# Kernel optimization log

Measured on AMD Instinct MI355X. Metric: run time of the kernel, lower is better.

The kernel has to match this reference:

```python
import jax, jax.numpy as jnp
from jax import lax
import numpy as np

NEIGHBORS = ((1, 3), (0, 2, 4), (1, 5), (0, 4, 6), (1, 3, 5, 7), (2, 4, 8), (3, 7), (4, 6, 8), (5, 7))
EDGE_SRC = np.array([s for t, ns in enumerate(NEIGHBORS) for s in ns])  # 25 edges
EDGE_DST = np.array([t for t, ns in enumerate(NEIGHBORS) for _ in ns])
NE = len(EDGE_SRC)  # 25
NG, SP = 9, 64      # num_grids, single_plane = 576 // 9
R, C_IN, C_OUT, ROI = 64, 256, 576, 14
GN_GROUPS = 36
EPS = 1e-5


def conv2d(x, w, b, stride, pad):
    y = lax.conv_general_dilated(x, w, (stride, stride), [(pad, pad), (pad, pad)],
                                 dimension_numbers=('NCHW', 'OIHW', 'NCHW'))
    return y + b[None, :, None, None]


def group_norm(x, groups, gamma, beta):
    B, C, H, W = x.shape
    xg = x.reshape(B, groups, -1)
    mu = xg.mean(-1, keepdims=True)
    var = xg.var(-1, keepdims=True)
    xn = ((xg - mu) / jnp.sqrt(var + EPS)).reshape(B, C, H, W)
    return xn * gamma[None, :, None, None] + beta[None, :, None, None]


def edge_conv(inp, dw_w, dw_b, pw_w, pw_b):
    # depthwise 5x5 (groups=SP) then pointwise 1x1
    y = lax.conv_general_dilated(inp, dw_w, (1, 1), [(2, 2), (2, 2)],
                                 dimension_numbers=('NCHW', 'OIHW', 'NCHW'),
                                 feature_group_count=SP) + dw_b[None, :, None, None]
    return jnp.einsum('bchw,oc->bohw', y, pw_w) + pw_b[None, :, None, None]


def deconv_grouped(x, w_t, b, groups):
    # torch ConvTranspose2d(k=4, s=2, p=1, groups) as lhs-dilated conv
    k, s, p = 4, 2, 1
    in_c, out_g = w_t.shape[0], w_t.shape[1]
    in_g = in_c // groups
    w = w_t.reshape(groups, in_g, out_g, k, k).transpose(0, 2, 1, 3, 4).reshape(groups * out_g, in_g, k, k)
    w = jnp.flip(w, (-2, -1))
    y = lax.conv_general_dilated(x, w, (1, 1), [(k - 1 - p, k - 1 - p)] * 2,
                                 lhs_dilation=(s, s),
                                 dimension_numbers=('NCHW', 'OIHW', 'NCHW'),
                                 feature_group_count=groups)
    return y + b[None, :, None, None]


def setup_inputs() -> dict:
    key = jax.random.key(0)
    ks = iter(jax.random.split(key, 32))
    n = lambda shape, s=0.02: jax.random.normal(next(ks), shape, jnp.float32) * s
    inp = {
        'x': jax.random.normal(next(ks), (R, C_IN, ROI, ROI), jnp.float32),
        'convs_w0': n((C_OUT, C_IN, 3, 3)),
        'convs_b0': n((C_OUT,)),
        'convs_w': n((7, C_OUT, C_OUT, 3, 3)),
        'convs_b': n((7, C_OUT)),
        'gn_gamma': jnp.ones((8, C_OUT), jnp.float32),
        'gn_beta': jnp.zeros((8, C_OUT), jnp.float32),
        'fo_dw_w': n((NE, SP, 1, 5, 5), 0.05),
        'fo_dw_b': n((NE, SP)),
        'fo_pw_w': n((NE, SP, SP), 0.05),
        'fo_pw_b': n((NE, SP)),
        'so_dw_w': n((NE, SP, 1, 5, 5), 0.05),
        'so_dw_b': n((NE, SP)),
        'so_pw_w': n((NE, SP, SP), 0.05),
        'so_pw_b': n((NE, SP)),
        'up1_w': n((C_OUT, SP, 4, 4), 0.01),
        'up1_b': jnp.zeros((C_OUT,), jnp.float32),
        'sbn1_gamma': jnp.ones((C_OUT,), jnp.float32),
        'sbn1_beta': jnp.zeros((C_OUT,), jnp.float32),
        'up2_w': n((C_OUT, 1, 4, 4), 0.01),
        'up2_b': jnp.full((NG,), -np.log(0.99 / 0.01), jnp.float32),
    }
    return inp


def reference(x, convs_w0, convs_b0, convs_w, convs_b, gn_gamma, gn_beta,
              fo_dw_w, fo_dw_b, fo_pw_w, fo_pw_b,
              so_dw_w, so_dw_b, so_pw_w, so_pw_b,
              up1_w, up1_b, sbn1_gamma, sbn1_beta, up2_w, up2_b):
    # dense conv stack: stride 2 first, then 7 stride-1 convs (GN + ReLU each)
    h = jax.nn.relu(group_norm(conv2d(x, convs_w0, convs_b0, 2, 1), GN_GROUPS, gn_gamma[0], gn_beta[0]))
    for i in range(7):
        h = jax.nn.relu(group_norm(conv2d(h, convs_w[i], convs_b[i], 1, 1),
                                   GN_GROUPS, gn_gamma[i + 1], gn_beta[i + 1]))
    B, _, Hh, Wh = h.shape  # [B, 576, 7, 7]
    xg = h.reshape(B, NG, SP, Hh, Wh).transpose(1, 0, 2, 3, 4)  # [9, B, 64, 7, 7]
    # first-order message passing over 25 grid edges
    msgs1 = jax.vmap(edge_conv)(xg[EDGE_SRC], fo_dw_w, fo_dw_b, fo_pw_w, fo_pw_b)
    first = xg + jax.ops.segment_sum(msgs1, EDGE_DST, num_segments=NG)
    # second-order message passing (sources are first-order features)
    msgs2 = jax.vmap(edge_conv)(first[EDGE_SRC], so_dw_w, so_dw_b, so_pw_w, so_pw_b)
    second = xg + jax.ops.segment_sum(msgs2, EDGE_DST, num_segments=NG)
    x2 = second.transpose(1, 0, 2, 3, 4).reshape(B, NG * SP, Hh, Wh)

    def head(t):
        t = deconv_grouped(t, up1_w, up1_b, NG)           # [B, 576, 14, 14]
        t = jax.nn.relu(group_norm(t, NG, sbn1_gamma, sbn1_beta))
        return deconv_grouped(t, up2_w, up2_b, NG)        # [B, 9, 28, 28]

    return (head(h), head(x2))
```

## Files before the change

kernel.cpp:

```cpp
#include <hip/hip_runtime.h>
#include <hip/hip_bf16.h>

#define BB 64
#define CIN 256
#define CC 576
#define NGR 9
#define SPC 64
#define HW7 49
#define HW14 196
#define HW28 784

__device__ __constant__ int EDGE_SRC_C[24] = {1,3, 0,2,4, 1,5, 0,4,6, 1,3,5,7, 2,4,8, 3,7, 4,6,8, 5,7};
__device__ __constant__ int EDGE_OFF_C[9]  = {0,2,5,7,10,14,17,19,22};
__device__ __constant__ int EDGE_CNT_C[9]  = {2,3,2,3,4,3,2,3,2};

static __device__ __forceinline__ float bf2f(__hip_bfloat16 v){ return __bfloat162float(v); }
static __device__ __forceinline__ __hip_bfloat16 f2bf(float v){ return __float2bfloat16(v); }
static __device__ __forceinline__ float ldin(const void* p, size_t i, int isbf){
  return isbf ? bf2f(((const __hip_bfloat16*)p)[i]) : ((const float*)p)[i];
}

using bfrag = __attribute__((ext_vector_type(8))) short;
using f32x4 = __attribute__((ext_vector_type(4))) float;

__global__ void detect_kernel(const unsigned short* xs, int* flag) {
  if (threadIdx.x==0 && blockIdx.x==0) {
    int plaus = 0;
    for (int i=0;i<64;i++){
      unsigned short u = xs[2*i];
      int e = (u>>7)&0xFF;
      if (e>=100 && e<=140) plaus++;
    }
    *flag = (plaus >= 40) ? 1 : 0;
  }
}

__global__ __launch_bounds__(256) void xcvt_kernel(
    const void* __restrict__ x, const int* __restrict__ flagp,
    __hip_bfloat16* __restrict__ act0) {
  const int b = blockIdx.x, icb = blockIdx.y, pxb = blockIdx.z, t = threadIdx.x;
  const int isbf = *flagp;
  __shared__ float lds[32][29];
  for (int idx=t; idx<32*28; idx+=256){
    int i = idx/28, j = idx - i*28;
    lds[i][j] = ldin(x, ((size_t)b*CIN + icb*32+i)*HW14 + pxb*28 + j, isbf);
  }
  __syncthreads();
  for (int idx=t; idx<28*32; idx+=256){
    int j = idx >> 5, i = idx & 31;
    act0[((size_t)b*HW14 + pxb*28 + j)*CIN + icb*32 + i] = f2bf(lds[i][j]);
  }
}

__global__ __launch_bounds__(256) void wcvt0_kernel(
    const void* __restrict__ w, const int* __restrict__ flagp,
    __hip_bfloat16* __restrict__ dst) {
  const int oc = blockIdx.x, t = threadIdx.x;
  const int isbf = *flagp;
  __shared__ float lds[2304];
  for (int idx=t; idx<2304; idx+=256)
    lds[idx] = ldin(w, (size_t)oc*2304 + idx, isbf);
  __syncthreads();
  for (int idx=t; idx<2304; idx+=256){
    int koff = idx >> 8, rem = idx & 255;
    int icb = rem >> 5, ici = rem & 31;
    dst[(((size_t)koff*8 + icb)*CC + oc)*32 + ici] = f2bf(lds[rem*9 + koff]);
  }
}

__global__ __launch_bounds__(256) void wcvtL_kernel(
    const void* __restrict__ w, int li, const int* __restrict__ flagp,
    __hip_bfloat16* __restrict__ dst) {
  const int oc = blockIdx.x, t = threadIdx.x;
  const int isbf = *flagp;
  __shared__ float lds[5184];
  for (int idx=t; idx<5184; idx+=256)
    lds[idx] = ldin(w, ((size_t)li*CC + oc)*5184 + idx, isbf);
  __syncthreads();
  for (int idx=t; idx<5184; idx+=256){
    int koff = idx / 576, rem = idx - koff*576;
    int icb = rem >> 5, ici = rem & 31;
    dst[(((size_t)koff*18 + icb)*CC + oc)*32 + ici] = f2bf(lds[rem*9 + koff]);
  }
}

static __device__ __forceinline__ void epilogue_gn(
    float* s_out, float* s_stats, const f32x4 (&acc)[2][2],
    int wm, int wn, int ln, int quad, int t,
    const void* bias, int bias_off,
    const void* gamma, const void* beta, int goff,
    int nbb, int isbf, int b,
    __hip_bfloat16* __restrict__ out)
{
  __syncthreads();
  #pragma unroll
  for (int nf=0; nf<2; nf++){
    int chl = wn*32 + nf*16 + ln;
    float bv = ldin(bias, (size_t)bias_off + nbb + chl, isbf);
    #pragma unroll
    for (int mf=0; mf<2; mf++){
      #pragma unroll
      for (int r=0; r<4; r++){
        int px = wm*32 + mf*16 + quad*4 + r;
        s_out[chl*65 + px] = acc[mf][nf][r] + bv;
      }
    }
  }
  __syncthreads();
  {
    int wv = t >> 6, l = t & 63;
    float s=0.f, ss=0.f;
    for (int j=l; j<784; j+=64){
      int cq = j/49, px = j - cq*49;
      float v = s_out[(wv*16+cq)*65 + px];
      s += v; ss += v*v;
    }
    #pragma unroll
    for (int o=32;o>0;o>>=1){ s+=__shfl_down(s,o); ss+=__shfl_down(ss,o); }
    if (l==0){
      float mean=s/784.f, var=ss/784.f-mean*mean;
      s_stats[wv*2]=mean; s_stats[wv*2+1]=rsqrtf(fmaxf(var,0.f)+1e-5f);
    }
  }
  __syncthreads();
  for (int idx=t; idx<392; idx+=256){
    int px = idx>>3, ck = idx&7;
    alignas(16) __hip_bfloat16 tmp[8];
    #pragma unroll
    for (int u=0;u<8;u++){
      int chl = ck*8+u;
      int gi = chl>>4;
      float ga = ldin(gamma, (size_t)goff + nbb + chl, isbf);
      float be = ldin(beta,  (size_t)goff + nbb + chl, isbf);
      float v = (s_out[chl*65+px]-s_stats[gi*2])*s_stats[gi*2+1]*ga + be;
      tmp[u] = f2bf(fmaxf(v,0.f));
    }
    *(bfrag*)(out + ((size_t)b*64+px)*CC + nbb + ck*8) = *(const bfrag*)tmp;
  }
}

__global__ __launch_bounds__(256) void conv3_v3_kernel(
    const __hip_bfloat16* __restrict__ A,
    const __hip_bfloat16* __restrict__ Wb,
    const void* __restrict__ bias, int bias_off,
    const void* __restrict__ gamma, const void* __restrict__ beta, int goff,
    const int* __restrict__ flagp,
    __hip_bfloat16* __restrict__ out) {
  const int t = threadIdx.x;
  const int l = t & 63, w = t >> 6;
  const int wm = w & 1, wn = (w >> 1) & 1;
  const int ln = l & 15, quad = l >> 4;
  const int b = blockIdx.x, nbb = blockIdx.y*32;
  const int isbf = *flagp;

  __shared__ alignas(16) char smem[8320];
  __shared__ float s_stats[4];
  __hip_bfloat16* sA0 = (__hip_bfloat16*)smem;
  __hip_bfloat16* sA1 = (__hip_bfloat16*)(smem + 4000);
  float* s_out = (float*)smem;

  if (t < 8){
    bfrag z = {0,0,0,0,0,0,0,0};
    __hip_bfloat16* sb = (t<4)? sA0 : sA1;
    *(bfrag*)(sb + 49*40 + (t&3)*8) = z;
  }

  int r0a[9], r1a[9];
  {
    int p0 = wm*32 + ln, p1 = p0+16;
    int y0=p0/7, x0=p0-y0*7, y1=p1/7, x1=p1-y1*7;
    bool v0=p0<49, v1=p1<49;
    #pragma unroll
    for (int koff=0;koff<9;koff++){
      int dy=koff/3-1, dx=koff-(koff/3)*3-1;
      int sy0=y0+dy,sx0=x0+dx, sy1=y1+dy,sx1=x1+dx;
      r0a[koff] = (v0&&sy0>=0&&sy0<7&&sx0>=0&&sx0<7)? sy0*7+sx0 : 49;
      r1a[koff] = (v1&&sy1>=0&&sy1<7&&sx1>=0&&sx1<7)? sy1*7+sx1 : 49;
    }
  }

  f32x4 acc2[2];
  acc2[0] = (f32x4){0.f,0.f,0.f,0.f};
  acc2[1] = (f32x4){0.f,0.f,0.f,0.f};

  const int px_s = t>>2, ic_s = (t&3)*8;
  const __hip_bfloat16* Abase = A + ((size_t)b*64 + px_s)*CC + ic_s;

  if (t<196) *(bfrag*)(sA0 + px_s*40 + ic_s) = *(const bfrag*)(Abase);
  __syncthreads();

  const int nidx = nbb + wn*16 + ln;
  for (int icb=0; icb<18; icb++){
    __hip_bfloat16* curb = (icb&1)? sA1 : sA0;
    if (icb<17 && t<196){
      __hip_bfloat16* nxtb = (icb&1)? sA0 : sA1;
      *(bfrag*)(nxtb + px_s*40 + ic_s) = *(const bfrag*)(Abase + (icb+1)*32);
    }
    const __hip_bfloat16* wpB = Wb + (size_t)icb*18432 + (size_t)nidx*32 + quad*8;
    #pragma unroll
    for (int koff=0;koff<9;koff++){
      bfrag a0 = *(const bfrag*)(curb + r0a[koff]*40 + quad*8);
      bfrag a1 = *(const bfrag*)(curb + r1a[koff]*40 + quad*8);
      bfrag b0 = *(const bfrag*)(wpB + (size_t)koff*331776);
      acc2[0] = __builtin_amdgcn_mfma_f32_16x16x32_bf16(a0, b0, acc2[0], 0,0,0);
      acc2[1] = __builtin_amdgcn_mfma_f32_16x16x32_bf16(a1, b0, acc2[1], 0,0,0);
    }
    __syncthreads();
  }

  {
    const int chl = wn*16 + ln;
    float bv = ldin(bias, (size_t)bias_off + nbb + chl, isbf);
    #pragma unroll
    for (int mf=0; mf<2; mf++)
      #pragma unroll
      for (int r=0;r<4;r++){
        int px = wm*32 + mf*16 + quad*4 + r;
        s_out[chl*65 + px] = acc2[mf][r] + bv;
      }
  }
  __syncthreads();
  {
    int wv = t >> 6, l2 = t & 63;
    if (wv < 2){
      float s=0.f, ss=0.f;
      for (int j=l2; j<784; j+=64){
        int cq = j/49, px = j - cq*49;
        float v = s_out[(wv*16+cq)*65 + px];
        s += v; ss += v*v;
      }
      #pragma unroll
      for (int o=32;o>0;o>>=1){ s+=__shfl_down(s,o); ss+=__shfl_down(ss,o); }
      if (l2==0){
        float mean=s/784.f, var=ss/784.f-mean*mean;
        s_stats[wv*2]=mean; s_stats[wv*2+1]=rsqrtf(fmaxf(var,0.f)+1e-5f);
      }
    }
  }
  __syncthreads();
  if (t < 196){
    int px = t>>2, ck = t&3;
    alignas(16) __hip_bfloat16 tmp[8];
    #pragma unroll
    for (int u=0;u<8;u++){
      int chl = ck*8+u;
      int gi = chl>>4;
      float ga = ldin(gamma, (size_t)goff + nbb + chl, isbf);
      float be = ldin(beta,  (size_t)goff + nbb + chl, isbf);
      float v = (s_out[chl*65+px]-s_stats[gi*2])*s_stats[gi*2+1]*ga + be;
      tmp[u] = f2bf(fmaxf(v,0.f));
    }
    *(bfrag*)(out + ((size_t)b*64+px)*CC + nbb + ck*8) = *(const bfrag*)tmp;
  }
}

__global__ __launch_bounds__(256) void conv0_fused_kernel(
    const __hip_bfloat16* __restrict__ A,
    const __hip_bfloat16* __restrict__ Wb,
    const void* __restrict__ bias,
    const void* __restrict__ gamma, const void* __restrict__ beta,
    const int* __restrict__ flagp,
    __hip_bfloat16* __restrict__ out) {
  const int t = threadIdx.x;
  const int l = t & 63, w = t >> 6;
  const int wm = w & 1, wn = w >> 1;
  const int ln = l & 15, quad = l >> 4;
  const int b = blockIdx.x, nbb = blockIdx.y*64;

  __shared__ alignas(16) __hip_bfloat16 sC[197*40];
  __shared__ alignas(16) float s_out_arr[64*65];
  __shared__ float s_stats[8];

  if (t < 4){
    bfrag z = {0,0,0,0,0,0,0,0};
    *(bfrag*)(sC + 196*40 + t*8) = z;
  }

  int yy[2], xx[2]; bool pv[2];
  #pragma unroll
  for (int mf=0; mf<2; mf++){
    int p = wm*32 + mf*16 + ln;
    pv[mf] = p<49; yy[mf]=p/7; xx[mf]=p-yy[mf]*7;
  }

  f32x4 acc[2][2];
  #pragma unroll
  for (int i=0;i<2;i++)
    #pragma unroll
    for (int j=0;j<2;j++) acc[i][j] = (f32x4){0.f,0.f,0.f,0.f};

  for (int icb=0; icb<8; icb++){
    __syncthreads();
    for (int idx=t*8; idx<6272; idx+=2048){
      int px = idx>>5, ic = idx&31;
      *(bfrag*)(sC + px*40 + ic) = *(const bfrag*)(A + ((size_t)b*196+px)*256 + icb*32 + ic);
    }
    __syncthreads();
    for (int koff=0; koff<9; koff++){
      const int dy = koff/3 - 1, dx = koff - (koff/3)*3 - 1;
      int sy0=2*yy[0]+dy, sx0=2*xx[0]+dx;
      int r0 = (pv[0]&&sy0>=0&&sy0<14&&sx0>=0&&sx0<14) ? sy0*14+sx0 : 196;
      int sy1=2*yy[1]+dy, sx1=2*xx[1]+dx;
      int r1 = (pv[1]&&sy1>=0&&sy1<14&&sx1>=0&&sx1<14) ? sy1*14+sx1 : 196;
      bfrag a0 = *(const bfrag*)(sC + r0*40 + quad*8);
      bfrag a1 = *(const bfrag*)(sC + r1*40 + quad*8);
      const __hip_bfloat16* wp = Wb + ((size_t)(koff*8+icb)*576 + nbb + wn*32 + ln)*32 + quad*8;
      bfrag b0 = *(const bfrag*)(wp);
      bfrag b1 = *(const bfrag*)(wp + 16*32);
      acc[0][0] = __builtin_amdgcn_mfma_f32_16x16x32_bf16(a0, b0, acc[0][0], 0,0,0);
      acc[1][0] = __builtin_amdgcn_mfma_f32_16x16x32_bf16(a1, b0, acc[1][0], 0,0,0);
      acc[0][1] = __builtin_amdgcn_mfma_f32_16x16x32_bf16(a0, b1, acc[0][1], 0,0,0);
      acc[1][1] = __builtin_amdgcn_mfma_f32_16x16x32_bf16(a1, b1, acc[1][1], 0,0,0);
    }
  }

  epilogue_gn(s_out_arr, s_stats, acc, wm, wn, ln, quad, t,
              bias, 0, gamma, beta, 0, nbb, *flagp, b, out);
}

__global__ __launch_bounds__(256) void dw_edge_kernel(
    const __hip_bfloat16* __restrict__ F,
    const void* __restrict__ dw_w,
    const void* __restrict__ dw_b,
    const int* __restrict__ flagp,
    __hip_bfloat16* __restrict__ Y) {
  const int b = blockIdx.x, e = blockIdx.y, t = threadIdx.x;
  const int isbf = *flagp;
  const int src = EDGE_SRC_C[e];
  __shared__ alignas(16) __hip_bfloat16 sA[50*72];
  for (int idx=t; idx<400; idx+=256){
    if (idx < 392){
      int px = idx>>3, ic = (idx&7)*8;
      *(bfrag*)(sA + px*72 + ic) = *(const bfrag*)(F + ((size_t)b*64+px)*CC + src*64 + ic);
    } else {
      bfrag z = {0,0,0,0,0,0,0,0};
      *(bfrag*)(sA + 49*72 + (idx-392)*8) = z;
    }
  }
  __syncthreads();
  const int ch = t & 63, wv = t >> 6;
  float wd[25];
  #pragma unroll
  for (int j=0;j<25;j++) wd[j] = ldin(dw_w, (size_t)e*1600 + ch*25 + j, isbf);
  float dwb = ldin(dw_b, e*64 + ch, isbf);
  for (int px=wv; px<49; px+=4){
    int oy=px/7, ox=px-oy*7;
    float a = dwb;
    #pragma unroll
    for (int u=0;u<5;u++){
      int py = oy+u-2;
      bool vy = (py>=0)&&(py<7);
      #pragma unroll
      for (int v=0;v<5;v++){
        int pxx = ox+v-2;
        int r = (vy && pxx>=0 && pxx<7) ? py*7+pxx : 49;
        a += bf2f(sA[r*72 + ch]) * wd[u*5+v];
      }
    }
    Y[((size_t)(e*64+b)*49 + px)*64 + ch] = f2bf(a);
  }
}

__global__ __launch_bounds__(256) void pwpack_kernel(
    const void* __restrict__ pw_fo, const void* __restrict__ pw_so,
    const int* __restrict__ flagp,
    __hip_bfloat16* __restrict__ dfo, __hip_bfloat16* __restrict__ dso) {
  const int e = blockIdx.x, t = threadIdx.x;
  const int isbf = *flagp;
  for (int idx=t; idx<4096; idx+=256){
    dfo[(size_t)e*4096+idx] = f2bf(ldin(pw_fo, (size_t)e*4096+idx, isbf));
    dso[(size_t)e*4096+idx] = f2bf(ldin(pw_so, (size_t)e*4096+idx, isbf));
  }
}

__global__ __launch_bounds__(256) void pw_seg_kernel(
    const __hip_bfloat16* __restrict__ Y,
    const __hip_bfloat16* __restrict__ base,
    const __hip_bfloat16* __restrict__ pwb,
    const void* __restrict__ pw_b,
    const int* __restrict__ flagp,
    __hip_bfloat16* __restrict__ out) {
  const int t = threadIdx.x, l = t & 63, w = t >> 6;
  const int wm = w & 1, wn = w >> 1;
  const int ln = l & 15, quad = l >> 4;
  const int dst = blockIdx.y;
  const int mt = blockIdx.x*64 + wm*32;
  const int m0 = mt + ln, m1 = m0 + 16;

  f32x4 acc[2][2];
  #pragma unroll
  for (int i=0;i<2;i++)
    #pragma unroll
    for (int j=0;j<2;j++) acc[i][j] = (f32x4){0.f,0.f,0.f,0.f};

  const int eoff = EDGE_OFF_C[dst], ecnt = EDGE_CNT_C[dst];
  for (int k=0;k<ecnt;k++){
    const __hip_bfloat16* Ye = Y + (size_t)(eoff+k)*3136*64;
    const __hip_bfloat16* pe = pwb + (size_t)(eoff+k)*4096;
    #pragma unroll
    for (int ks=0; ks<2; ks++){
      const int kq = ks*32 + quad*8;
      bfrag a0 = *(const bfrag*)(Ye + (size_t)m0*64 + kq);
      bfrag a1 = *(const bfrag*)(Ye + (size_t)m1*64 + kq);
      bfrag b0 = *(const bfrag*)(pe + (wn*32+ln)*64 + kq);
      bfrag b1 = *(const bfrag*)(pe + (wn*32+ln+16)*64 + kq);
      acc[0][0] = __builtin_amdgcn_mfma_f32_16x16x32_bf16(a0, b0, acc[0][0], 0,0,0);
      acc[1][0] = __builtin_amdgcn_mfma_f32_16x16x32_bf16(a1, b0, acc[1][0], 0,0,0);
      acc[0][1] = __builtin_amdgcn_mfma_f32_16x16x32_bf16(a0, b1, acc[0][1], 0,0,0);
      acc[1][1] = __builtin_amdgcn_mfma_f32_16x16x32_bf16(a1, b1, acc[1][1], 0,0,0);
    }
  }

  const int isbf = *flagp;
  #pragma unroll
  for (int nf=0; nf<2; nf++){
    int n = wn*32 + nf*16 + ln;
    float pbs = 0.f;
    for (int k=0;k<ecnt;k++) pbs += ldin(pw_b, (size_t)(eoff+k)*64 + n, isbf);
    #pragma unroll
    for (int mf=0; mf<2; mf++){
      #pragma unroll
      for (int r=0; r<4; r++){
        int m = mt + mf*16 + quad*4 + r;
        int bb = m/49, px = m - bb*49;
        size_t oi = ((size_t)bb*64 + px)*CC + dst*64 + n;
        out[oi] = f2bf(bf2f(base[oi]) + acc[mf][nf][r] + pbs);
      }
    }
  }
}

__global__ __launch_bounds__(256) void wpack_dc1_kernel(
    const void* __restrict__ w1, const int* __restrict__ flagp,
    __hip_bfloat16* __restrict__ dst) {
  const int gtap = blockIdx.x, t = threadIdx.x;
  const int isbf = *flagp;
  const int g = gtap >> 4, tap = gtap & 15;
  for (int idx=t; idx<64*64; idx+=256){
    int oc = idx >> 6, ic = idx & 63;
    dst[((size_t)gtap*64 + oc)*64 + ic] =
        f2bf(ldin(w1, ((size_t)(g*64+ic)*64 + oc)*16 + tap, isbf));
  }
}

__global__ __launch_bounds__(256) void dc1_mfma_kernel(
    const __hip_bfloat16* __restrict__ H,
    const __hip_bfloat16* __restrict__ Wp,
    const void* __restrict__ b1,
    const int* __restrict__ flagp,
    __hip_bfloat16* __restrict__ mid) {
  const int tid = threadIdx.x;
  const int l = tid & 63;
  const int w = tid >> 6;
  const int wm = w & 1, wn = w >> 1;
  const int g = blockIdx.y;
  const int mt = blockIdx.x*64 + wm*32;
  const int nb = wn*32;
  const int ln = l & 15;
  const int quad = l >> 4;

  int bb[2], iy_t[2][4], ix_t[2][4]; bool vy[2][4], vx[2][4];
  #pragma unroll
  for (int mf=0; mf<2; mf++){
    int m = mt + mf*16 + ln;
    int b = m/196, px = m - b*196;
    bb[mf] = b;
    int oy = px/14, ox = px - oy*14;
    #pragma unroll
    for (int k=0;k<4;k++){
      int ny = oy+1-k; vy[mf][k] = (ny>=0) && !(ny&1) && (ny>>1)<7; iy_t[mf][k]=(ny>>1)*7;
      int nx = ox+1-k; vx[mf][k] = (nx>=0) && !(nx&1) && (nx>>1)<7; ix_t[mf][k]=nx>>1;
    }
  }

  f32x4 acc[2][2];
  #pragma unroll
  for (int i=0;i<2;i++)
    #pragma unroll
    for (int j=0;j<2;j++) acc[i][j] = (f32x4){0.f,0.f,0.f,0.f};
  const bfrag zf = {0,0,0,0,0,0,0,0};

  for (int tap=0; tap<16; tap++){
    const int ky = tap>>2, kx = tap&3;
    int ipx[2]; bool tv[2];
    #pragma unroll
    for (int mf=0; mf<2; mf++){
      tv[mf] = vy[mf][ky] && vx[mf][kx];
      ipx[mf] = iy_t[mf][ky] + ix_t[mf][kx];
    }
    const __hip_bfloat16* wrow = Wp + (((size_t)(g*16+tap)*64 + nb + ln)*64);
    #pragma unroll
    for (int half=0; half<2; half++){
      const int icq = half*32 + quad*8;
      bfrag a0 = tv[0] ? *(const bfrag*)(H + ((size_t)(bb[0]*64 + ipx[0]))*CC + g*64 + icq) : zf;
      bfrag a1 = tv[1] ? *(const bfrag*)(H + ((size_t)(bb[1]*64 + ipx[1]))*CC + g*64 + icq) : zf;
      bfrag b0 = *(const bfrag*)(wrow + icq);
      bfrag b1v = *(const bfrag*)(wrow + 16*64 + icq);
      acc[0][0] = __builtin_amdgcn_mfma_f32_16x16x32_bf16(a0, b0,  acc[0][0], 0,0,0);
      acc[1][0] = __builtin_amdgcn_mfma_f32_16x16x32_bf16(a1, b0,  acc[1][0], 0,0,0);
      acc[0][1] = __builtin_amdgcn_mfma_f32_16x16x32_bf16(a0, b1v, acc[0][1], 0,0,0);
      acc[1][1] = __builtin_amdgcn_mfma_f32_16x16x32_bf16(a1, b1v, acc[1][1], 0,0,0);
    }
  }

  const int isbf = *flagp;
  #pragma unroll
  for (int nf=0; nf<2; nf++){
    int n = g*64 + nb + nf*16 + ln;
    float bv = ldin(b1, n, isbf);
    #pragma unroll
    for (int mf=0; mf<2; mf++){
      #pragma unroll
      for (int r=0; r<4; r++){
        int m = mt + mf*16 + quad*4 + r;
        int b = m/196, px = m - b*196;
        mid[((size_t)b*196 + px)*CC + n] = f2bf(acc[mf][nf][r] + bv);
      }
    }
  }
}

__global__ __launch_bounds__(256) void dc2gn_kernel(
    const __hip_bfloat16* __restrict__ mid,
    const void* __restrict__ gamma, const void* __restrict__ beta,
    const void* __restrict__ w2,
    const void* __restrict__ b2,
    const int* __restrict__ flagp,
    void* __restrict__ outp,
    size_t out_elem_off) {
  const int isbf = *flagp;
  const int b=blockIdx.x, g=blockIdx.y, z=blockIdx.z, t=threadIdx.x;
  const int c = t & 63;
  __shared__ __hip_bfloat16 s_mid[64*113];
  __shared__ float s_w2[64][17];
  __shared__ float red[8]; __shared__ float stats[2];
  const __hip_bfloat16* mbase = mid + (size_t)b*196*CC + g*64;

  {
    float s=0.f, ss=0.f;
    for (int idx=t; idx<12544; idx+=256){
      int ipx = idx>>6;
      float v = bf2f(mbase[(size_t)ipx*CC + (idx&63)]);
      s+=v; ss+=v*v;
    }
    #pragma unroll
    for (int o=32;o>0;o>>=1){ s+=__shfl_down(s,o); ss+=__shfl_down(ss,o); }
    int wid=t>>6;
    if ((t&63)==0){ red[wid]=s; red[4+wid]=ss; }
  }
  for (int idx=t; idx<1024; idx+=256)
    s_w2[idx>>4][idx&15] = ldin(w2, (g*SPC + (idx>>4))*16 + (idx&15), isbf);
  __syncthreads();
  if (t==0){
    float S=red[0]+red[1]+red[2]+red[3];
    float SS=red[4]+red[5]+red[6]+red[7];
    float mean=S/12544.f, var=SS/12544.f-mean*mean;
    stats[0]=mean; stats[1]=rsqrtf(fmaxf(var,0.f)+1e-5f);
  }
  __syncthreads();
  const float mean=stats[0], inv=stats[1];
  const int rbase = z*6;
  {
    float ga = ldin(gamma, g*SPC+c, isbf), be = ldin(beta, g*SPC+c, isbf);
    for (int idx=t; idx<7168; idx+=256){
      int pl = idx>>6;
      int ipx = (rbase + pl/14)*14 + (pl%14);
      float v = (bf2f(mbase[(size_t)ipx*CC + c])-mean)*inv*ga + be;
      s_mid[c*113 + pl] = f2bf(fmaxf(v, 0.f));
    }
  }
  __syncthreads();
  float b2v = ldin(b2, g, isbf);
  for (int p=t; p<392; p+=256){
    int oyl = p/28, ox = p - oyl*28;
    int oy = z*14 + oyl;
    float a = b2v;
    for (int cc=0; cc<64; cc++){
      #pragma unroll
      for (int kyi=0;kyi<2;kyi++){
        int ky=((oy+1)&1)+2*kyi; int ny=oy+1-ky;
        if (ny>=0){
          int iy=ny>>1;
          if (iy<14){
            int li = iy - rbase;
            #pragma unroll
            for (int kxi=0;kxi<2;kxi++){
              int kx=((ox+1)&1)+2*kxi; int nx=ox+1-kx;
              if (nx>=0){
                int ix=nx>>1;
                if (ix<14) a += bf2f(s_mid[cc*113 + li*14 + ix])*s_w2[cc][ky*4+kx];
              }
            }
          }
        }
      }
    }
    size_t oidx = out_elem_off + ((size_t)b*NGR+g)*HW28 + oy*28 + ox;
    if (isbf) ((__hip_bfloat16*)outp)[oidx] = f2bf(a);
    else      ((float*)outp)[oidx] = a;
  }
}

extern "C" void kernel_launch(void* const* d_in, const int* in_sizes, int n_in,
                              void* d_out, int out_size, void* d_ws, size_t ws_size,
                              hipStream_t stream) {
  const void* x        = d_in[0];
  const void* convs_w0 = d_in[1];
  const void* convs_b0 = d_in[2];
  const void* convs_w  = d_in[3];
  const void* convs_b  = d_in[4];
  const void* gn_gamma = d_in[5];
  const void* gn_beta  = d_in[6];
  const void* fo_dw_w  = d_in[7];
  const void* fo_dw_b  = d_in[8];
  const void* fo_pw_w  = d_in[9];
  const void* fo_pw_b  = d_in[10];
  const void* so_dw_w  = d_in[11];
  const void* so_dw_b  = d_in[12];
  const void* so_pw_w  = d_in[13];
  const void* so_pw_b  = d_in[14];
  const void* up1_w    = d_in[15];
  const void* up1_b    = d_in[16];
  const void* sbn_g    = d_in[17];
  const void* sbn_b    = d_in[18];
  const void* up2_w    = d_in[19];
  const void* up2_b    = d_in[20];
  (void)in_sizes; (void)n_in; (void)out_size; (void)ws_size;

  int* flag = (int*)d_ws;
  char* wsb = (char*)d_ws + 16;
  __hip_bfloat16* act0   = (__hip_bfloat16*)(wsb);
  __hip_bfloat16* wbuf   = (__hip_bfloat16*)(wsb + 6422528);
  __hip_bfloat16* actA   = (__hip_bfloat16*)(wsb + 12394496);
  __hip_bfloat16* actB   = (__hip_bfloat16*)(wsb + 17113088);
  __hip_bfloat16* bufF   = (__hip_bfloat16*)(wsb + 21831680);
  __hip_bfloat16* secN   = (__hip_bfloat16*)(wsb + 26550272);
  __hip_bfloat16* wpack  = (__hip_bfloat16*)(wsb + 31268864);
  __hip_bfloat16* pwbF   = (__hip_bfloat16*)(wsb + 32448512);
  __hip_bfloat16* pwbS   = (__hip_bfloat16*)(wsb + 32645120);
  __hip_bfloat16* Y      = (__hip_bfloat16*)(wsb);
  __hip_bfloat16* mid    = (__hip_bfloat16*)(wsb);

  detect_kernel<<<1, 1, 0, stream>>>((const unsigned short*)x, flag);

  xcvt_kernel<<<dim3(BB,8,7), 256, 0, stream>>>(x, flag, act0);
  wcvt0_kernel<<<CC, 256, 0, stream>>>(convs_w0, flag, wbuf);
  conv0_fused_kernel<<<dim3(64,9), 256, 0, stream>>>(
      act0, wbuf, convs_b0, gn_gamma, gn_beta, flag, actA);

  __hip_bfloat16* cur = actA; __hip_bfloat16* nxt = actB;
  for (int i=0;i<7;i++){
    wcvtL_kernel<<<CC, 256, 0, stream>>>(convs_w, i, flag, wbuf);
    conv3_v3_kernel<<<dim3(64,18), 256, 0, stream>>>(
        cur, wbuf, convs_b, i*CC, gn_gamma, gn_beta, (i+1)*CC, flag, nxt);
    __hip_bfloat16* tmp=cur; cur=nxt; nxt=tmp;
  }

  wpack_dc1_kernel<<<144, 256, 0, stream>>>(up1_w, flag, wpack);
  pwpack_kernel<<<24, 256, 0, stream>>>(fo_pw_w, so_pw_w, flag, pwbF, pwbS);

  dw_edge_kernel<<<dim3(BB,24), 256, 0, stream>>>(cur, fo_dw_w, fo_dw_b, flag, Y);
  pw_seg_kernel<<<dim3(49,NGR), 256, 0, stream>>>(Y, cur, pwbF, fo_pw_b, flag, bufF);
  dw_edge_kernel<<<dim3(BB,24), 256, 0, stream>>>(bufF, so_dw_w, so_dw_b, flag, Y);
  pw_seg_kernel<<<dim3(49,NGR), 256, 0, stream>>>(Y, cur, pwbS, so_pw_b, flag, secN);

  dc1_mfma_kernel<<<dim3(196,NGR), 256, 0, stream>>>(cur, wpack, up1_b, flag, mid);
  dc2gn_kernel<<<dim3(BB,NGR,2), 256, 0, stream>>>(mid, sbn_g, sbn_b, up2_w, up2_b, flag, d_out, 0);
  dc1_mfma_kernel<<<dim3(196,NGR), 256, 0, stream>>>(secN, wpack, up1_b, flag, mid);
  dc2gn_kernel<<<dim3(BB,NGR,2), 256, 0, stream>>>(mid, sbn_g, sbn_b, up2_w, up2_b, flag, d_out, (size_t)BB*NGR*HW28);
}
```

Before: 1.076 ms.

## Decompose first deconv into stride-2 output parity classes with LDS-staged input

Replaces the 16-tap transposed-conv GEMM with a per-output-parity (sub-pixel) formulation, so each block handles one of four output phase classes and runs only the 4 taps that contribute instead of all 16 with zero-masked loads. Input activations for the block's batches are staged into shared memory with a zero pad row, so A fragments come from LDS rather than scattered global loads. This cuts MFMA work by about four times for this stage. The cost is a shared-memory staging step with a barrier, and output writes scattered across parity positions.

```diff
diff --git a/kernel.cpp b/kernel.cpp
--- a/kernel.cpp
+++ b/kernel.cpp
@@ -443,33 +443,53 @@
   }
 }
 
-__global__ __launch_bounds__(256) void dc1_mfma_kernel(
+__global__ __launch_bounds__(256) void dc1_cls_kernel(
     const __hip_bfloat16* __restrict__ H,
     const __hip_bfloat16* __restrict__ Wp,
     const void* __restrict__ b1,
     const int* __restrict__ flagp,
     __hip_bfloat16* __restrict__ mid) {
-  const int tid = threadIdx.x;
-  const int l = tid & 63;
-  const int w = tid >> 6;
+  const int t = threadIdx.x;
+  const int l = t & 63, w = t >> 6;
   const int wm = w & 1, wn = w >> 1;
-  const int g = blockIdx.y;
-  const int mt = blockIdx.x*64 + wm*32;
-  const int nb = wn*32;
-  const int ln = l & 15;
-  const int quad = l >> 4;
-
-  int bb[2], iy_t[2][4], ix_t[2][4]; bool vy[2][4], vx[2][4];
+  const int ln = l & 15, quad = l >> 4;
+  const int Mt = blockIdx.x;
+  const int cls = blockIdx.y;
+  const int g = blockIdx.z;
+  const int ry = cls >> 1, rx = cls & 1;
+  const int b0 = (Mt*64)/49;
+
+  __shared__ alignas(16) __hip_bfloat16 sX[3*50*72];
+
+  {
+    const bfrag z = {0,0,0,0,0,0,0,0};
+    for (int idx=t; idx<1200; idx+=256){
+      int bi = idx/400, rem = idx - bi*400;
+      int p = rem>>3, ch = (rem&7)*8;
+      bfrag v = z;
+      if (p < 49 && (b0+bi) < 64)
+        v = *(const bfrag*)(H + ((size_t)((b0+bi)*64) + p)*CC + g*64 + ch);
+      *(bfrag*)(sX + (bi*50+p)*72 + ch) = v;
+    }
+  }
+
+  int aoff[2][4];
   #pragma unroll
   for (int mf=0; mf<2; mf++){
-    int m = mt + mf*16 + ln;
-    int b = m/196, px = m - b*196;
-    bb[mf] = b;
-    int oy = px/14, ox = px - oy*14;
-    #pragma unroll
-    for (int k=0;k<4;k++){
-      int ny = oy+1-k; vy[mf][k] = (ny>=0) && !(ny&1) && (ny>>1)<7; iy_t[mf][k]=(ny>>1)*7;
-      int nx = ox+1-k; vx[mf][k] = (nx>=0) && !(nx&1) && (nx>>1)<7; ix_t[mf][k]=nx>>1;
+    int m = Mt*64 + wm*32 + mf*16 + ln;
+    int b = m/49, p = m - b*49;
+    int py = p/7, pxx = p - py*7;
+    int bloc = b - b0;
+    #pragma unroll
+    for (int kyi=0;kyi<2;kyi++){
+      int iy = py + ry - kyi;
+      bool vy = (iy>=0)&&(iy<7);
+      #pragma unroll
+      for (int kxi=0;kxi<2;kxi++){
+        int ix = pxx + rx - kxi;
+        int r = (vy && ix>=0 && ix<7) ? iy*7+ix : 49;
+        aoff[mf][kyi*2+kxi] = (bloc*50 + r)*72 + quad*8;
+      }
     }
   }
 
@@ -478,44 +498,54 @@
   for (int i=0;i<2;i++)
     #pragma unroll
     for (int j=0;j<2;j++) acc[i][j] = (f32x4){0.f,0.f,0.f,0.f};
-  const bfrag zf = {0,0,0,0,0,0,0,0};
-
-  for (int tap=0; tap<16; tap++){
-    const int ky = tap>>2, kx = tap&3;
-    int ipx[2]; bool tv[2];
-    #pragma unroll
-    for (int mf=0; mf<2; mf++){
-      tv[mf] = vy[mf][ky] && vx[mf][kx];
-      ipx[mf] = iy_t[mf][ky] + ix_t[mf][kx];
-    }
-    const __hip_bfloat16* wrow = Wp + (((size_t)(g*16+tap)*64 + nb + ln)*64);
-    #pragma unroll
-    for (int half=0; half<2; half++){
-      const int icq = half*32 + quad*8;
-      bfrag a0 = tv[0] ? *(const bfrag*)(H + ((size_t)(bb[0]*64 + ipx[0]))*CC + g*64 + icq) : zf;
-      bfrag a1 = tv[1] ? *(const bfrag*)(H + ((size_t)(bb[1]*64 + ipx[1]))*CC + g*64 + icq) : zf;
-      bfrag b0 = *(const bfrag*)(wrow + icq);
-      bfrag b1v = *(const bfrag*)(wrow + 16*64 + icq);
-      acc[0][0] = __builtin_amdgcn_mfma_f32_16x16x32_bf16(a0, b0,  acc[0][0], 0,0,0);
-      acc[1][0] = __builtin_amdgcn_mfma_f32_16x16x32_bf16(a1, b0,  acc[1][0], 0,0,0);
-      acc[0][1] = __builtin_amdgcn_mfma_f32_16x16x32_bf16(a0, b1v, acc[0][1], 0,0,0);
-      acc[1][1] = __builtin_amdgcn_mfma_f32_16x16x32_bf16(a1, b1v, acc[1][1], 0,0,0);
-    }
-  }
-
-  const int isbf = *flagp;
-  #pragma unroll
-  for (int nf=0; nf<2; nf++){
-    int n = g*64 + nb + nf*16 + ln;
-    float bv = ldin(b1, n, isbf);
-    #pragma unroll
-    for (int mf=0; mf<2; mf++){
-      #pragma unroll
-      for (int r=0; r<4; r++){
-        int m = mt + mf*16 + quad*4 + r;
-        int b = m/196, px = m - b*196;
-        mid[((size_t)b*196 + px)*CC + n] = f2bf(acc[mf][nf][r] + bv);
-      }
+
+  __syncthreads();
+
+  const int ky0 = 1-ry, kx0 = 1-rx;
+  #pragma unroll
+  for (int kyi=0;kyi<2;kyi++){
+    #pragma unroll
+    for (int kxi=0;kxi<2;kxi++){
+      const int tap = (ky0+2*kyi)*4 + (kx0+2*kxi);
+      const __hip_bfloat16* wb =
+          Wp + ((size_t)(g*16+tap)*64 + wn*32 + ln)*64 + quad*8;
+      const int ao0 = aoff[0][kyi*2+kxi], ao1 = aoff[1][kyi*2+kxi];
+      #pragma unroll
+      for (int half=0; half<2; half++){
+        bfrag a0 = *(const bfrag*)(sX + ao0 + half*32);
+        bfrag a1 = *(const bfrag*)(sX + ao1 + half*32);
+        bfrag w0 = *(const bfrag*)(wb + half*32);
+        bfrag w1 = *(const bfrag*)(wb + 16*64 + half*32);
+        acc[0][0] = __builtin_amdgcn_mfma_f32_16x16x32_bf16(a0, w0, acc[0][0], 0,0,0);
+        acc[1][0] = __builtin_amdgcn_mfma_f32_16x16x32_bf16(a1, w0, acc[1][0], 0,0,0);
+        acc[0][1] = __builtin_amdgcn_mfma_f32_16x16x32_bf16(a0, w1, acc[0][1], 0,0,0);
+        acc[1][1] = __builtin_amdgcn_mfma_f32_16x16x32_bf16(a1, w1, acc[1][1], 0,0,0);
+      }
+    }
+  }
+
+  const int isbf = *flagp;
+  size_t ob[2][4];
+  #pragma unroll
+  for (int mf=0;mf<2;mf++){
+    #pragma unroll
+    for (int r=0;r<4;r++){
+      int m = Mt*64 + wm*32 + mf*16 + quad*4 + r;
+      int b = m/49, p = m - b*49;
+      int py = p/7, pxx = p - py*7;
+      int oy = 2*py + ry, ox = 2*pxx + rx;
+      ob[mf][r] = ((size_t)b*196 + oy*14 + ox)*CC + g*64;
+    }
+  }
+  #pragma unroll
+  for (int nf=0;nf<2;nf++){
+    int n = wn*32 + nf*16 + ln;
+    float bv = ldin(b1, g*64 + n, isbf);
+    #pragma unroll
+    for (int mf=0;mf<2;mf++){
+      #pragma unroll
+      for (int r=0;r<4;r++)
+        mid[ob[mf][r] + n] = f2bf(acc[mf][nf][r] + bv);
     }
   }
 }
@@ -664,8 +694,8 @@
   dw_edge_kernel<<<dim3(BB,24), 256, 0, stream>>>(bufF, so_dw_w, so_dw_b, flag, Y);
   pw_seg_kernel<<<dim3(49,NGR), 256, 0, stream>>>(Y, cur, pwbS, so_pw_b, flag, secN);
 
-  dc1_mfma_kernel<<<dim3(196,NGR), 256, 0, stream>>>(cur, wpack, up1_b, flag, mid);
+  dc1_cls_kernel<<<dim3(49,4,NGR), 256, 0, stream>>>(cur, wpack, up1_b, flag, mid);
   dc2gn_kernel<<<dim3(BB,NGR,2), 256, 0, stream>>>(mid, sbn_g, sbn_b, up2_w, up2_b, flag, d_out, 0);
-  dc1_mfma_kernel<<<dim3(196,NGR), 256, 0, stream>>>(secN, wpack, up1_b, flag, mid);
+  dc1_cls_kernel<<<dim3(49,4,NGR), 256, 0, stream>>>(secN, wpack, up1_b, flag, mid);
   dc2gn_kernel<<<dim3(BB,NGR,2), 256, 0, stream>>>(mid, sbn_g, sbn_b, up2_w, up2_b, flag, d_out, (size_t)BB*NGR*HW28);
 }
```

After: 965.9 us. 10.3% less time.
